# Performance work log

Hardware: AMD Instinct MI355X
Metric: run time of the kernel (lower is better)

Reference implementation:

```python
import jax, jax.numpy as jnp
import numpy as np

B, N, D = 1024, 100000, 512


def setup_inputs() -> dict:
    key = jax.random.key(0)
    k1, k2, k3 = jax.random.split(key, 3)
    x_t = jax.random.normal(k1, (B, D), dtype=jnp.float32)
    # keep t away from 0/1 so b_t = 1 - t is well conditioned
    t = jax.random.uniform(k2, (B,), dtype=jnp.float32, minval=0.05, maxval=0.95)
    dataset = jax.random.normal(k3, (N, D), dtype=jnp.float32)
    return {"x_t": x_t, "t": t, "dataset": dataset}


def reference(x_t, t, dataset):
    # Straight-line AffineInterp: a_t = t, b_t = 1 - t, dot_a = 1, dot_b = -1.
    # Original detaches coeffs (detach=True).
    a_t = jax.lax.stop_gradient(t)
    b_t = jax.lax.stop_gradient(1.0 - t)
    dot_a_t = jnp.ones_like(a_t)
    dot_b_t = -jnp.ones_like(b_t)

    dataset_norm = jnp.sum(dataset * dataset, axis=1)          # (N,)
    term_1 = jnp.sum(x_t * x_t, axis=1)                        # (B,)
    term_2 = jnp.einsum('bd,nd->bn', x_t, dataset)             # (B, N)

    # ||x_t - a_t * x1||^2 expanded, scaled by -1/(2 b_t^2)
    logit = (term_1[:, None]
             - 2.0 * a_t[:, None] * term_2
             + (a_t * a_t)[:, None] * dataset_norm[None, :])
    logit = (-1.0 / (2.0 * b_t * b_t))[:, None] * logit        # (B, N)

    prob = jax.nn.softmax(logit, axis=1)                       # (B, N)
    data_coeff = dot_a_t - a_t * dot_b_t / b_t                 # (B,)
    prob = prob * data_coeff[:, None]

    weighted_dataset = jnp.einsum('bn,nd->bd', prob, dataset)  # (B, D)
    v = (dot_b_t / b_t)[:, None] * x_t + weighted_dataset
    return v
```

## Files before the change

### kernel.cpp

```cpp
#include <hip/hip_runtime.h>
#include <math.h>

#define B_SZ 1024
#define N_SZ 100000
#define D_SZ 512
#define NBLK 3125

typedef __attribute__((ext_vector_type(8))) short short8;
typedef __attribute__((ext_vector_type(16))) float float16;

__device__ __forceinline__ unsigned f2bf(float x) {
    unsigned u = __float_as_uint(x);
    u += 0x7FFFu + ((u >> 16) & 1u);
    return u >> 16;
}
__device__ __forceinline__ float bf2f(unsigned h) {
    return __uint_as_float(h << 16);
}

__global__ __launch_bounds__(256) void pre_kernel(
    const float* __restrict__ ds, const float* __restrict__ x_t,
    short* __restrict__ Yh, short* __restrict__ Yl, short* __restrict__ Yt,
    short* __restrict__ Xh, short* __restrict__ Xl, float* __restrict__ norms)
{
    __shared__ unsigned short YS[32 * 512];
    const int bx = blockIdx.x, tid = threadIdx.x;
    if (bx < NBLK) {
        const int row = tid >> 3, seg = tid & 7;
        const size_t g = (size_t)(bx * 32 + row) * 512 + seg * 64;
        const int ls = row * 512 + seg * 64;
        float nrm = 0.f;
        #pragma unroll
        for (int i = 0; i < 16; i++) {
            float4 v = *(const float4*)(ds + g + i * 4);
            nrm += v.x*v.x + v.y*v.y + v.z*v.z + v.w*v.w;
            unsigned h0 = f2bf(v.x), h1 = f2bf(v.y), h2 = f2bf(v.z), h3 = f2bf(v.w);
            unsigned l0 = f2bf(v.x - bf2f(h0)), l1 = f2bf(v.y - bf2f(h1));
            unsigned l2 = f2bf(v.z - bf2f(h2)), l3 = f2bf(v.w - bf2f(h3));
            uint2 hw = make_uint2(h0 | (h1 << 16), h2 | (h3 << 16));
            uint2 lw = make_uint2(l0 | (l1 << 16), l2 | (l3 << 16));
            *(uint2*)(Yh + g + i * 4) = hw;
            *(uint2*)(Yl + g + i * 4) = lw;
            *(uint2*)(YS + ls + i * 4) = hw;
        }
        nrm += __shfl_xor(nrm, 1, 64);
        nrm += __shfl_xor(nrm, 2, 64);
        nrm += __shfl_xor(nrm, 4, 64);
        if ((tid & 7) == 0) norms[bx * 32 + row] = nrm;
        __syncthreads();
        #pragma unroll
        for (int r = 0; r < 2; r++) {
            const int d = tid + r * 256;
            unsigned w[16];
            #pragma unroll
            for (int j = 0; j < 16; j++) {
                unsigned lo = YS[(2 * j) * 512 + d];
                unsigned hi = YS[(2 * j + 1) * 512 + d];
                w[j] = lo | (hi << 16);
            }
            uint4* dst = (uint4*)(Yt + (size_t)bx * 16384 + d * 32);
            dst[0] = make_uint4(w[0], w[1], w[2], w[3]);
            dst[1] = make_uint4(w[4], w[5], w[6], w[7]);
            dst[2] = make_uint4(w[8], w[9], w[10], w[11]);
            dst[3] = make_uint4(w[12], w[13], w[14], w[15]);
        }
    } else {
        const int xb = bx - NBLK;
        #pragma unroll
        for (int k = 0; k < 16; k++) {
            const size_t i4 = (size_t)xb * 4096 + k * 256 + tid;
            float4 v = *(const float4*)(x_t + i4 * 4);
            unsigned h0 = f2bf(v.x), h1 = f2bf(v.y), h2 = f2bf(v.z), h3 = f2bf(v.w);
            unsigned l0 = f2bf(v.x - bf2f(h0)), l1 = f2bf(v.y - bf2f(h1));
            unsigned l2 = f2bf(v.z - bf2f(h2)), l3 = f2bf(v.w - bf2f(h3));
            *(uint2*)(Xh + i4 * 4) = make_uint2(h0 | (h1 << 16), h2 | (h3 << 16));
            *(uint2*)(Xl + i4 * 4) = make_uint2(l0 | (l1 << 16), l2 | (l3 << 16));
        }
    }
}

__global__ __launch_bounds__(512, 2) void attn_kernel(
    const float* __restrict__ t,
    const short* __restrict__ Xh, const short* __restrict__ Xl,
    const short* __restrict__ Yh, const short* __restrict__ Yl,
    const short* __restrict__ Yt, const float* __restrict__ norms,
    float* __restrict__ m_part, float* __restrict__ l_part,
    float* __restrict__ acc_part, int chunk)
{
    __shared__ short YhL[32 * 512];
    __shared__ short YlL[32 * 512];
    __shared__ float slots[4 * 64 * 33];
    __shared__ float Pbuf[64 * 36];
    __shared__ float c1A[64], c2A[64], mAs[64], lAs[64], alA[64];
    __shared__ float nrmL[32];

    const int tid = threadIdx.x;
    const int wave = tid >> 6, lane = tid & 63;
    const int half = lane >> 5, l31 = lane & 31;
    const int qb = blockIdx.x * 64;
    const int s = blockIdx.y;
    const int n0s = s * chunk;
    const int n1 = min(N_SZ, n0s + chunk);
    const int numTiles = (n1 - n0s + 31) >> 5;

    if (tid < 64) {
        float tv = t[qb + tid];
        float bt = 1.0f - tv;
        float i2 = 1.0f / (2.0f * bt * bt);
        c1A[tid] = 2.0f * tv * i2;
        c2A[tid] = tv * tv * i2;
        mAs[tid] = -1e30f;
        lAs[tid] = 0.0f;
        alA[tid] = 0.0f;
    }
    __syncthreads();

    if (wave < 4) {
        short8 XF[2][8][2];
        #pragma unroll
        for (int qt = 0; qt < 2; qt++)
            #pragma unroll
            for (int kc = 0; kc < 8; kc++) {
                size_t off = (size_t)(qb + qt * 32 + l31) * 512 + wave * 128 + kc * 16 + half * 8;
                XF[qt][kc][0] = *(const short8*)(Xh + off);
                XF[qt][kc][1] = *(const short8*)(Xl + off);
            }

        for (int it = 0; it <= numTiles; ++it) {
            if (it < numTiles) {
                int n0 = n0s + it * 32;
                #pragma unroll
                for (int j = 0; j < 8; j++) {
                    int r = wave * 8 + j;
                    int gr = n0 + r;
                    if (gr < n1) {
                        const short* gh = Yh + (size_t)gr * 512 + lane * 8;
                        const short* gl = Yl + (size_t)gr * 512 + lane * 8;
                        __builtin_amdgcn_global_load_lds(
                            (const __attribute__((address_space(1))) unsigned int*)gh,
                            (__attribute__((address_space(3))) unsigned int*)&YhL[r * 512], 16, 0, 0);
                        __builtin_amdgcn_global_load_lds(
                            (const __attribute__((address_space(1))) unsigned int*)gl,
                            (__attribute__((address_space(3))) unsigned int*)&YlL[r * 512], 16, 0, 0);
                    } else {
                        short8 z;
                        #pragma unroll
                        for (int e = 0; e < 8; e++) z[e] = 0;
                        *(short8*)(&YhL[r * 512 + lane * 8]) = z;
                        *(short8*)(&YlL[r * 512 + lane * 8]) = z;
                    }
                }
                if (wave == 0 && lane < 32)
                    nrmL[lane] = (n0 + lane < n1) ? norms[n0 + lane] : 1e30f;
            }
            __syncthreads();

            if (it < numTiles) {
                float16 S0, S1;
                #pragma unroll
                for (int e = 0; e < 16; e++) { S0[e] = 0.f; S1[e] = 0.f; }
                #pragma unroll
                for (int kc = 0; kc < 8; kc++) {
                    const int koff = wave * 128 + kc * 16 + half * 8;
                    short8 Ah = *(const short8*)(YhL + l31 * 512 + koff);
                    short8 Al = *(const short8*)(YlL + l31 * 512 + koff);
                    S0 = __builtin_amdgcn_mfma_f32_32x32x16_bf16(Ah, XF[0][kc][0], S0, 0, 0, 0);
                    S0 = __builtin_amdgcn_mfma_f32_32x32x16_bf16(Ah, XF[0][kc][1], S0, 0, 0, 0);
                    S0 = __builtin_amdgcn_mfma_f32_32x32x16_bf16(Al, XF[0][kc][0], S0, 0, 0, 0);
                    S1 = __builtin_amdgcn_mfma_f32_32x32x16_bf16(Ah, XF[1][kc][0], S1, 0, 0, 0);
                    S1 = __builtin_amdgcn_mfma_f32_32x32x16_bf16(Ah, XF[1][kc][1], S1, 0, 0, 0);
                    S1 = __builtin_amdgcn_mfma_f32_32x32x16_bf16(Al, XF[1][kc][0], S1, 0, 0, 0);
                }
                float* sb = &slots[wave * 2112];
                #pragma unroll
                for (int qt = 0; qt < 2; qt++) {
                    float* rowp = sb + (qt * 32 + l31) * 33;
                    #pragma unroll
                    for (int r = 0; r < 16; r++) {
                        int n = (r & 3) + 8 * (r >> 2) + 4 * half;
                        rowp[n] = qt ? S1[r] : S0[r];
                    }
                }
            }
            __syncthreads();

            if (it < numTiles) {
                int ql = lane >> 2, nq = lane & 3;
                int q = wave * 16 + ql;
                float c1q = c1A[q], c2q = c2A[q];
                float lg[8];
                float mt = -1e30f;
                #pragma unroll
                for (int j = 0; j < 8; j++) {
                    int n = nq * 8 + j;
                    float dd = slots[q * 33 + n] + slots[2112 + q * 33 + n]
                             + slots[4224 + q * 33 + n] + slots[6336 + q * 33 + n];
                    lg[j] = c1q * dd - c2q * nrmL[n];
                    mt = fmaxf(mt, lg[j]);
                }
                mt = fmaxf(mt, __shfl_xor(mt, 1, 64));
                mt = fmaxf(mt, __shfl_xor(mt, 2, 64));
                float mo = mAs[q];
                float mn = fmaxf(mo, mt);
                float al = __expf(mo - mn);
                float ls = 0.f;
                #pragma unroll
                for (int j = 0; j < 8; j++) {
                    float p = __expf(lg[j] - mn);
                    Pbuf[q * 36 + nq * 8 + j] = p;
                    ls += p;
                }
                ls += __shfl_xor(ls, 1, 64);
                ls += __shfl_xor(ls, 2, 64);
                if (nq == 0) {
                    mAs[q] = mn;
                    lAs[q] = lAs[q] * al + ls;
                    alA[q] = al;
                }
            }
            __syncthreads();
        }
        if (tid < 64) {
            m_part[(size_t)s * B_SZ + qb + tid] = mAs[tid];
            l_part[(size_t)s * B_SZ + qb + tid] = lAs[tid];
        }
    } else {
        const int dbase = (wave - 4) * 128;
        float16 O[4][2];
        #pragma unroll
        for (int dt = 0; dt < 4; dt++)
            #pragma unroll
            for (int qt = 0; qt < 2; qt++)
                #pragma unroll
                for (int e = 0; e < 16; e++) O[dt][qt][e] = 0.f;

        for (int it = 0; it <= numTiles; ++it) {
            __syncthreads();
            if (it > 0) {
                int blk = (n0s + (it - 1) * 32) >> 5;
                const short* yb = Yt + (size_t)blk * 16384;
                float al0 = alA[l31], al1 = alA[32 + l31];
                #pragma unroll
                for (int dt = 0; dt < 4; dt++) {
                    O[dt][0] *= al0;
                    O[dt][1] *= al1;
                }
                short8 AF[4][2];
                #pragma unroll
                for (int dt = 0; dt < 4; dt++)
                    #pragma unroll
                    for (int kc = 0; kc < 2; kc++)
                        AF[dt][kc] = *(const short8*)(yb + (dbase + dt * 32 + l31) * 32 + kc * 16 + half * 8);
                short8 BF[2][2];
                #pragma unroll
                for (int qt = 0; qt < 2; qt++)
                    #pragma unroll
                    for (int kc = 0; kc < 2; kc++) {
                        const float* pr = &Pbuf[(qt * 32 + l31) * 36 + kc * 16 + half * 8];
                        float4 pa = *(const float4*)pr;
                        float4 pb = *(const float4*)(pr + 4);
                        short8 b;
                        b[0] = (short)f2bf(pa.x); b[1] = (short)f2bf(pa.y);
                        b[2] = (short)f2bf(pa.z); b[3] = (short)f2bf(pa.w);
                        b[4] = (short)f2bf(pb.x); b[5] = (short)f2bf(pb.y);
                        b[6] = (short)f2bf(pb.z); b[7] = (short)f2bf(pb.w);
                        BF[qt][kc] = b;
                    }
                #pragma unroll
                for (int dt = 0; dt < 4; dt++)
                    #pragma unroll
                    for (int qt = 0; qt < 2; qt++)
                        #pragma unroll
                        for (int kc = 0; kc < 2; kc++)
                            O[dt][qt] = __builtin_amdgcn_mfma_f32_32x32x16_bf16(
                                AF[dt][kc], BF[qt][kc], O[dt][qt], 0, 0, 0);
            }
            __syncthreads();
            __syncthreads();
        }
        #pragma unroll
        for (int dt = 0; dt < 4; dt++)
            #pragma unroll
            for (int qt = 0; qt < 2; qt++) {
                int q = qb + qt * 32 + l31;
                float* op = acc_part + ((size_t)s * B_SZ + q) * D_SZ + dbase + dt * 32 + 4 * half;
                #pragma unroll
                for (int rg = 0; rg < 4; rg++) {
                    float4 v = make_float4(O[dt][qt][4 * rg], O[dt][qt][4 * rg + 1],
                                           O[dt][qt][4 * rg + 2], O[dt][qt][4 * rg + 3]);
                    *(float4*)(op + 8 * rg) = v;
                }
            }
    }
}

__global__ __launch_bounds__(256) void combine_kernel(
    const float* __restrict__ x_t, const float* __restrict__ t,
    const float* __restrict__ m_part, const float* __restrict__ l_part,
    const float* __restrict__ acc_part, float* __restrict__ out, int nsplit)
{
    int q = blockIdx.x;
    int tid = threadIdx.x;
    float M = -1e30f;
    for (int s = 0; s < nsplit; s++) M = fmaxf(M, m_part[(size_t)s * B_SZ + q]);
    float L = 0.f;
    for (int s = 0; s < nsplit; s++)
        L += l_part[(size_t)s * B_SZ + q] * __expf(m_part[(size_t)s * B_SZ + q] - M);

    float tv = t[q];
    float bt = 1.0f - tv;
    float coeff = 1.0f + tv / bt;
    float invb = 1.0f / bt;
    float invL = 1.0f / L;

    int d = tid * 2;
    float2 w = make_float2(0.f, 0.f);
    for (int s = 0; s < nsplit; s++) {
        float sc = __expf(m_part[(size_t)s * B_SZ + q] - M);
        float2 av = *(const float2*)(acc_part + ((size_t)s * B_SZ + q) * D_SZ + d);
        w.x += sc * av.x; w.y += sc * av.y;
    }
    float2 xv = *(const float2*)(x_t + (size_t)q * D_SZ + d);
    float2 o;
    o.x = -invb * xv.x + coeff * w.x * invL;
    o.y = -invb * xv.y + coeff * w.y * invL;
    *(float2*)(out + (size_t)q * D_SZ + d) = o;
}

extern "C" void kernel_launch(void* const* d_in, const int* in_sizes, int n_in,
                              void* d_out, int out_size, void* d_ws, size_t ws_size,
                              hipStream_t stream) {
    const float* x_t = (const float*)d_in[0];
    const float* t   = (const float*)d_in[1];
    const float* ds  = (const float*)d_in[2];
    float* out = (float*)d_out;

    short* wsS = (short*)d_ws;
    short* Yh = wsS;
    short* Yl = wsS + 51200000;
    short* Yt = wsS + 102400000;
    short* Xh = wsS + 153600000;
    short* Xl = wsS + 154124288;
    float* fbase = (float*)((char*)d_ws + 309297152);
    float* norms = fbase;
    int nsplit = 16;
    while (nsplit > 1 &&
           309697152ULL + (size_t)nsplit * 1024 * 4 * (2 + 512) > ws_size)
        nsplit >>= 1;
    float* m_part = fbase + 100000;
    float* l_part = m_part + (size_t)nsplit * B_SZ;
    float* acc    = l_part + (size_t)nsplit * B_SZ;
    int chunk = 32 * ((N_SZ + 32 * nsplit - 1) / (32 * nsplit));

    pre_kernel<<<dim3(NBLK + 32), dim3(256), 0, stream>>>(ds, x_t, Yh, Yl, Yt, Xh, Xl, norms);
    attn_kernel<<<dim3(16, nsplit), dim3(512), 0, stream>>>(
        t, Xh, Xl, Yh, Yl, Yt, norms, m_part, l_part, acc, chunk);
    combine_kernel<<<dim3(B_SZ), dim3(256), 0, stream>>>(
        x_t, t, m_part, l_part, acc, out, nsplit);
}
```

Baseline: 1.282 ms.

## Halve query tile to 32 rows and raise occupancy with compact shared layout

Each attention block now handles 32 queries instead of 64, doubling the grid and raising the launch-bounds occupancy target from 2 to 4 blocks per CU. The dataset tile is loaded into a fragment-ordered shared buffer, and the per-wave partial scores are summed with shared atomics into a single slot array instead of four. Probabilities are packed to bf16 once in the softmax stage rather than converted by every value-side wave. The goal is lower register and LDS pressure and more blocks in flight. The cost is that each dataset tile is read from global memory twice as many times. Shared atomics add contention, and the tail guard was removed, which assumes the chunk length is a multiple of 32.

```diff
diff --git a/kernel.cpp b/kernel.cpp
--- a/kernel.cpp
+++ b/kernel.cpp
@@ -79,7 +79,7 @@
     }
 }
 
-__global__ __launch_bounds__(512, 2) void attn_kernel(
+__global__ __launch_bounds__(512, 4) void attn_kernel(
     const float* __restrict__ t,
     const short* __restrict__ Xh, const short* __restrict__ Xl,
     const short* __restrict__ Yh, const short* __restrict__ Yl,
@@ -87,23 +87,21 @@
     float* __restrict__ m_part, float* __restrict__ l_part,
     float* __restrict__ acc_part, int chunk)
 {
-    __shared__ short YhL[32 * 512];
-    __shared__ short YlL[32 * 512];
-    __shared__ float slots[4 * 64 * 33];
-    __shared__ float Pbuf[64 * 36];
-    __shared__ float c1A[64], c2A[64], mAs[64], lAs[64], alA[64];
-    __shared__ float nrmL[32];
+    __shared__ short Ykm[32768];
+    __shared__ float slots[32 * 33];
+    __shared__ short Pb[4 * 32 * 8];
+    __shared__ float c1A[32], c2A[32], mAs[32], lAs[32], alA[32], nrmL[32];
 
     const int tid = threadIdx.x;
     const int wave = tid >> 6, lane = tid & 63;
     const int half = lane >> 5, l31 = lane & 31;
-    const int qb = blockIdx.x * 64;
+    const int qb = blockIdx.x * 32;
     const int s = blockIdx.y;
     const int n0s = s * chunk;
     const int n1 = min(N_SZ, n0s + chunk);
-    const int numTiles = (n1 - n0s + 31) >> 5;
-
-    if (tid < 64) {
+    const int numTiles = (n1 - n0s) >> 5;
+
+    if (tid < 32) {
         float tv = t[qb + tid];
         float bt = 1.0f - tv;
         float i2 = 1.0f / (2.0f * bt * bt);
@@ -113,105 +111,92 @@
         lAs[tid] = 0.0f;
         alA[tid] = 0.0f;
     }
+    for (int i = tid; i < 32 * 33; i += 512) slots[i] = 0.0f;
     __syncthreads();
 
     if (wave < 4) {
-        short8 XF[2][8][2];
-        #pragma unroll
-        for (int qt = 0; qt < 2; qt++)
-            #pragma unroll
-            for (int kc = 0; kc < 8; kc++) {
-                size_t off = (size_t)(qb + qt * 32 + l31) * 512 + wave * 128 + kc * 16 + half * 8;
-                XF[qt][kc][0] = *(const short8*)(Xh + off);
-                XF[qt][kc][1] = *(const short8*)(Xl + off);
-            }
+        const int w = wave;
+        short8 XF[8][2];
+        #pragma unroll
+        for (int kc = 0; kc < 8; kc++) {
+            size_t off = (size_t)(qb + l31) * 512 + w * 128 + kc * 16 + half * 8;
+            XF[kc][0] = *(const short8*)(Xh + off);
+            XF[kc][1] = *(const short8*)(Xl + off);
+        }
 
         for (int it = 0; it <= numTiles; ++it) {
             if (it < numTiles) {
                 int n0 = n0s + it * 32;
                 #pragma unroll
-                for (int j = 0; j < 8; j++) {
-                    int r = wave * 8 + j;
-                    int gr = n0 + r;
-                    if (gr < n1) {
-                        const short* gh = Yh + (size_t)gr * 512 + lane * 8;
-                        const short* gl = Yl + (size_t)gr * 512 + lane * 8;
-                        __builtin_amdgcn_global_load_lds(
-                            (const __attribute__((address_space(1))) unsigned int*)gh,
-                            (__attribute__((address_space(3))) unsigned int*)&YhL[r * 512], 16, 0, 0);
-                        __builtin_amdgcn_global_load_lds(
-                            (const __attribute__((address_space(1))) unsigned int*)gl,
-                            (__attribute__((address_space(3))) unsigned int*)&YlL[r * 512], 16, 0, 0);
-                    } else {
-                        short8 z;
-                        #pragma unroll
-                        for (int e = 0; e < 8; e++) z[e] = 0;
-                        *(short8*)(&YhL[r * 512 + lane * 8]) = z;
-                        *(short8*)(&YlL[r * 512 + lane * 8]) = z;
-                    }
-                }
-                if (wave == 0 && lane < 32)
-                    nrmL[lane] = (n0 + lane < n1) ? norms[n0 + lane] : 1e30f;
+                for (int j = 0; j < 16; j++) {
+                    int i = w * 16 + j;
+                    int g = (2 * i + half) & 63;
+                    const short* src = ((i >> 5) ? Yl : Yh)
+                                     + (size_t)(n0 + l31) * 512 + g * 8;
+                    __builtin_amdgcn_global_load_lds(
+                        (const __attribute__((address_space(1))) unsigned int*)src,
+                        (__attribute__((address_space(3))) unsigned int*)&Ykm[i * 512],
+                        16, 0, 0);
+                }
+                if (w == 0 && lane < 32) nrmL[lane] = norms[n0 + lane];
             }
             __syncthreads();
 
             if (it < numTiles) {
-                float16 S0, S1;
-                #pragma unroll
-                for (int e = 0; e < 16; e++) { S0[e] = 0.f; S1[e] = 0.f; }
+                float16 S;
+                #pragma unroll
+                for (int e = 0; e < 16; e++) S[e] = 0.f;
                 #pragma unroll
                 for (int kc = 0; kc < 8; kc++) {
-                    const int koff = wave * 128 + kc * 16 + half * 8;
-                    short8 Ah = *(const short8*)(YhL + l31 * 512 + koff);
-                    short8 Al = *(const short8*)(YlL + l31 * 512 + koff);
-                    S0 = __builtin_amdgcn_mfma_f32_32x32x16_bf16(Ah, XF[0][kc][0], S0, 0, 0, 0);
-                    S0 = __builtin_amdgcn_mfma_f32_32x32x16_bf16(Ah, XF[0][kc][1], S0, 0, 0, 0);
-                    S0 = __builtin_amdgcn_mfma_f32_32x32x16_bf16(Al, XF[0][kc][0], S0, 0, 0, 0);
-                    S1 = __builtin_amdgcn_mfma_f32_32x32x16_bf16(Ah, XF[1][kc][0], S1, 0, 0, 0);
-                    S1 = __builtin_amdgcn_mfma_f32_32x32x16_bf16(Ah, XF[1][kc][1], S1, 0, 0, 0);
-                    S1 = __builtin_amdgcn_mfma_f32_32x32x16_bf16(Al, XF[1][kc][0], S1, 0, 0, 0);
-                }
-                float* sb = &slots[wave * 2112];
-                #pragma unroll
-                for (int qt = 0; qt < 2; qt++) {
-                    float* rowp = sb + (qt * 32 + l31) * 33;
-                    #pragma unroll
-                    for (int r = 0; r < 16; r++) {
-                        int n = (r & 3) + 8 * (r >> 2) + 4 * half;
-                        rowp[n] = qt ? S1[r] : S0[r];
-                    }
+                    int g = w * 16 + kc * 2 + half;
+                    short8 Ah = *(const short8*)(Ykm + (g * 32 + l31) * 8);
+                    short8 Al = *(const short8*)(Ykm + 16384 + (g * 32 + l31) * 8);
+                    S = __builtin_amdgcn_mfma_f32_32x32x16_bf16(Ah, XF[kc][0], S, 0, 0, 0);
+                    S = __builtin_amdgcn_mfma_f32_32x32x16_bf16(Ah, XF[kc][1], S, 0, 0, 0);
+                    S = __builtin_amdgcn_mfma_f32_32x32x16_bf16(Al, XF[kc][0], S, 0, 0, 0);
+                }
+                float* rowp = slots + l31 * 33;
+                #pragma unroll
+                for (int r = 0; r < 16; r++) {
+                    int n = (r & 3) + 8 * (r >> 2) + 4 * half;
+                    atomicAdd(rowp + n, S[r]);
                 }
             }
             __syncthreads();
 
             if (it < numTiles) {
-                int ql = lane >> 2, nq = lane & 3;
-                int q = wave * 16 + ql;
+                int ql = lane >> 3, nq = lane & 7;
+                int q = w * 8 + ql;
                 float c1q = c1A[q], c2q = c2A[q];
-                float lg[8];
+                float lg[4];
                 float mt = -1e30f;
                 #pragma unroll
-                for (int j = 0; j < 8; j++) {
-                    int n = nq * 8 + j;
-                    float dd = slots[q * 33 + n] + slots[2112 + q * 33 + n]
-                             + slots[4224 + q * 33 + n] + slots[6336 + q * 33 + n];
+                for (int j = 0; j < 4; j++) {
+                    int n = nq * 4 + j;
+                    float dd = slots[q * 33 + n];
+                    slots[q * 33 + n] = 0.0f;
                     lg[j] = c1q * dd - c2q * nrmL[n];
                     mt = fmaxf(mt, lg[j]);
                 }
                 mt = fmaxf(mt, __shfl_xor(mt, 1, 64));
                 mt = fmaxf(mt, __shfl_xor(mt, 2, 64));
+                mt = fmaxf(mt, __shfl_xor(mt, 4, 64));
                 float mo = mAs[q];
                 float mn = fmaxf(mo, mt);
                 float al = __expf(mo - mn);
                 float ls = 0.f;
-                #pragma unroll
-                for (int j = 0; j < 8; j++) {
+                unsigned pk[4];
+                #pragma unroll
+                for (int j = 0; j < 4; j++) {
                     float p = __expf(lg[j] - mn);
-                    Pbuf[q * 36 + nq * 8 + j] = p;
                     ls += p;
+                    pk[j] = f2bf(p);
                 }
                 ls += __shfl_xor(ls, 1, 64);
                 ls += __shfl_xor(ls, 2, 64);
+                ls += __shfl_xor(ls, 4, 64);
+                uint2 wv = make_uint2(pk[0] | (pk[1] << 16), pk[2] | (pk[3] << 16));
+                *(uint2*)(Pb + ((nq >> 1) * 32 + q) * 8 + (nq & 1) * 4) = wv;
                 if (nq == 0) {
                     mAs[q] = mn;
                     lAs[q] = lAs[q] * al + ls;
@@ -220,77 +205,55 @@
             }
             __syncthreads();
         }
-        if (tid < 64) {
+        if (tid < 32) {
             m_part[(size_t)s * B_SZ + qb + tid] = mAs[tid];
             l_part[(size_t)s * B_SZ + qb + tid] = lAs[tid];
         }
     } else {
         const int dbase = (wave - 4) * 128;
-        float16 O[4][2];
+        float16 O[4];
         #pragma unroll
         for (int dt = 0; dt < 4; dt++)
             #pragma unroll
-            for (int qt = 0; qt < 2; qt++)
-                #pragma unroll
-                for (int e = 0; e < 16; e++) O[dt][qt][e] = 0.f;
+            for (int e = 0; e < 16; e++) O[dt][e] = 0.f;
 
         for (int it = 0; it <= numTiles; ++it) {
             __syncthreads();
             if (it > 0) {
                 int blk = (n0s + (it - 1) * 32) >> 5;
                 const short* yb = Yt + (size_t)blk * 16384;
-                float al0 = alA[l31], al1 = alA[32 + l31];
+                float al = alA[l31];
+                short8 BF[2];
+                #pragma unroll
+                for (int kc = 0; kc < 2; kc++)
+                    BF[kc] = *(const short8*)(Pb + ((kc * 2 + half) * 32 + l31) * 8);
+                #pragma unroll
+                for (int dt = 0; dt < 4; dt++) O[dt] *= al;
                 #pragma unroll
                 for (int dt = 0; dt < 4; dt++) {
-                    O[dt][0] *= al0;
-                    O[dt][1] *= al1;
-                }
-                short8 AF[4][2];
-                #pragma unroll
-                for (int dt = 0; dt < 4; dt++)
-                    #pragma unroll
-                    for (int kc = 0; kc < 2; kc++)
-                        AF[dt][kc] = *(const short8*)(yb + (dbase + dt * 32 + l31) * 32 + kc * 16 + half * 8);
-                short8 BF[2][2];
-                #pragma unroll
-                for (int qt = 0; qt < 2; qt++)
                     #pragma unroll
                     for (int kc = 0; kc < 2; kc++) {
-                        const float* pr = &Pbuf[(qt * 32 + l31) * 36 + kc * 16 + half * 8];
-                        float4 pa = *(const float4*)pr;
-                        float4 pb = *(const float4*)(pr + 4);
-                        short8 b;
-                        b[0] = (short)f2bf(pa.x); b[1] = (short)f2bf(pa.y);
-                        b[2] = (short)f2bf(pa.z); b[3] = (short)f2bf(pa.w);
-                        b[4] = (short)f2bf(pb.x); b[5] = (short)f2bf(pb.y);
-                        b[6] = (short)f2bf(pb.z); b[7] = (short)f2bf(pb.w);
-                        BF[qt][kc] = b;
+                        short8 AF = *(const short8*)(
+                            yb + (dbase + dt * 32 + l31) * 32 + kc * 16 + half * 8);
+                        O[dt] = __builtin_amdgcn_mfma_f32_32x32x16_bf16(
+                            AF, BF[kc], O[dt], 0, 0, 0);
                     }
-                #pragma unroll
-                for (int dt = 0; dt < 4; dt++)
-                    #pragma unroll
-                    for (int qt = 0; qt < 2; qt++)
-                        #pragma unroll
-                        for (int kc = 0; kc < 2; kc++)
-                            O[dt][qt] = __builtin_amdgcn_mfma_f32_32x32x16_bf16(
-                                AF[dt][kc], BF[qt][kc], O[dt][qt], 0, 0, 0);
-            }
-            __syncthreads();
-            __syncthreads();
-        }
-        #pragma unroll
-        for (int dt = 0; dt < 4; dt++)
+                }
+            }
+            __syncthreads();
+            __syncthreads();
+        }
+        #pragma unroll
+        for (int dt = 0; dt < 4; dt++) {
+            float* op = acc_part + ((size_t)s * B_SZ + qb + l31) * D_SZ
+                      + dbase + dt * 32 + 4 * half;
             #pragma unroll
-            for (int qt = 0; qt < 2; qt++) {
-                int q = qb + qt * 32 + l31;
-                float* op = acc_part + ((size_t)s * B_SZ + q) * D_SZ + dbase + dt * 32 + 4 * half;
-                #pragma unroll
-                for (int rg = 0; rg < 4; rg++) {
-                    float4 v = make_float4(O[dt][qt][4 * rg], O[dt][qt][4 * rg + 1],
-                                           O[dt][qt][4 * rg + 2], O[dt][qt][4 * rg + 3]);
-                    *(float4*)(op + 8 * rg) = v;
-                }
-            }
+            for (int rg = 0; rg < 4; rg++) {
+                float4 v = make_float4(O[dt][4 * rg], O[dt][4 * rg + 1],
+                                       O[dt][4 * rg + 2], O[dt][4 * rg + 3]);
+                *(float4*)(op + 8 * rg) = v;
+            }
+        }
     }
 }
 
@@ -353,7 +316,7 @@
     int chunk = 32 * ((N_SZ + 32 * nsplit - 1) / (32 * nsplit));
 
     pre_kernel<<<dim3(NBLK + 32), dim3(256), 0, stream>>>(ds, x_t, Yh, Yl, Yt, Xh, Xl, norms);
-    attn_kernel<<<dim3(16, nsplit), dim3(512), 0, stream>>>(
+    attn_kernel<<<dim3(B_SZ / 32, nsplit), dim3(512), 0, stream>>>(
         t, Xh, Xl, Yh, Yl, Yt, norms, m_part, l_part, acc, chunk);
     combine_kernel<<<dim3(B_SZ), dim3(256), 0, stream>>>(
         x_t, t, m_part, l_part, acc, out, nsplit);
```

After: 3.808 ms. +196.9%, slower.
